# Optimization experiments

Measured on AMD Instinct MI355X. Metric: run time of the kernel, lower is better.

The kernel has to match this reference:

```python
import jax, jax.numpy as jnp
import numpy as np

B, S, V, E = 64, 100, 20000, 128
U, I = 10000, 20000


def setup_inputs() -> dict:
    key = jax.random.key(0)
    ks = jax.random.split(key, 12)
    initrange = 0.1
    return {
        "attr_item": jax.random.randint(ks[0], (B, S), 0, V, dtype=jnp.int32),
        "attr_tf_item": jax.random.uniform(ks[1], (B, S), dtype=jnp.float32),
        "attr_lens_item": jax.random.randint(ks[2], (B,), 1, S + 1, dtype=jnp.int32),
        "item_ids": jax.random.randint(ks[3], (B,), 0, I, dtype=jnp.int32),
        "attr_user": jax.random.randint(ks[4], (B, S), 0, V, dtype=jnp.int32),
        "attr_tf_user": jax.random.uniform(ks[5], (B, S), dtype=jnp.float32),
        "attr_lens_user": jax.random.randint(ks[6], (B,), 1, S + 1, dtype=jnp.int32),
        "user_ids": jax.random.randint(ks[7], (B,), 0, U, dtype=jnp.int32),
        "W_item": jax.random.uniform(ks[8], (V, E), jnp.float32, -initrange, initrange),
        "W_user": jax.random.uniform(ks[9], (V, E), jnp.float32, -initrange, initrange),
        "user_emb": jax.random.uniform(ks[10], (U, E), jnp.float32, -initrange, initrange),
        "item_emb": jax.random.uniform(ks[11], (I, E), jnp.float32, -initrange, initrange),
    }


def _cluster_logits(attr_ids, attr_tf, attr_lens, W):
    # attr_ids: [B,S] int, attr_tf: [B,S] float, attr_lens: [B] int, W: [V,E]
    seq = attr_ids.shape[1]
    mask = (jnp.arange(seq)[None, :] < attr_lens[:, None]).astype(attr_tf.dtype)  # [B,S]
    emb = W[attr_ids]                                   # [B,S,E]
    scores = jnp.einsum("bse,ve->bsv", emb, W)          # [B,S,V]
    cw = jax.nn.softmax(scores, axis=1)                 # softmax over seq dim (dim=1 in torch)
    # Algebraically identical to the [B,S,V,E] broadcast-mul-sum in the original:
    # logits[b,v] = sum_s (tf*mask)[b,s] * cw[b,s,v] * scores[b,s,v]
    return jnp.einsum("bs,bsv,bsv->bv", attr_tf * mask, cw, scores)


def reference(attr_item, attr_tf_item, attr_lens_item, item_ids,
              attr_user, attr_tf_user, attr_lens_user, user_ids,
              W_item, W_user, user_emb, item_emb):
    logits = _cluster_logits(attr_item, attr_tf_item, attr_lens_item, W_item)
    logits = logits + _cluster_logits(attr_user, attr_tf_user, attr_lens_user, W_user)
    logits = logits + user_emb[user_ids] @ W_user.T     # [B,V]
    logits = logits + item_emb[item_ids] @ W_item.T     # [B,V]
    return logits
```

## Files before the change

kernel.cpp:

```cpp
#include <hip/hip_runtime.h>

#define VDIM 20000
#define EDIM 128
#define BATCH 64
#define SEQ 100
#define BN 96
#define NVT 209

typedef float f32x4 __attribute__((ext_vector_type(4)));
typedef short bf16x8 __attribute__((ext_vector_type(8)));
typedef unsigned short ushortx8 __attribute__((ext_vector_type(8)));

typedef __attribute__((address_space(1))) const unsigned int gas_u32;
typedef __attribute__((address_space(3))) unsigned int las_u32;

__device__ __forceinline__ void async16(unsigned short* lds, const unsigned short* g) {
  __builtin_amdgcn_global_load_lds((gas_u32*)g, (las_u32*)lds, 16, 0, 0);
}

__device__ __forceinline__ unsigned short f2bf(float f) {
  unsigned u = __builtin_bit_cast(unsigned, f);
  u += 0x7FFFu + ((u >> 16) & 1u);
  return (unsigned short)(u >> 16);
}

__global__ void prep_kernel(const float* __restrict__ Wi, const float* __restrict__ Wu,
                            const int* __restrict__ attr_item, const int* __restrict__ attr_user,
                            const int* __restrict__ item_ids, const int* __restrict__ user_ids,
                            const float* __restrict__ item_emb, const float* __restrict__ user_emb,
                            unsigned short* __restrict__ wbf, unsigned short* __restrict__ abf) {
  const int bid = blockIdx.x, t = threadIdx.x;
  if (bid < 2500) {
    const int c = bid & 1;
    const float* src = c ? Wu : Wi;
    unsigned short* dst = wbf + (size_t)c * (VDIM * EDIM);
    const int i0 = ((bid >> 1) * 256 + t) * 8;
    float4 a = *(const float4*)(src + i0);
    float4 b = *(const float4*)(src + i0 + 4);
    ushortx8 o;
    o[0] = f2bf(a.x); o[1] = f2bf(a.y); o[2] = f2bf(a.z); o[3] = f2bf(a.w);
    o[4] = f2bf(b.x); o[5] = f2bf(b.y); o[6] = f2bf(b.z); o[7] = f2bf(b.w);
    *(ushortx8*)(dst + i0) = o;
  } else {
    const int g = bid - 2500;
    const int b = g & 63, c = g >> 6;
    const int r = t >> 1, h = t & 1;
    const int* ids = c ? attr_user : attr_item;
    const float* W = c ? Wu : Wi;
    const float* demb = c ? user_emb : item_emb;
    const int* dids = c ? user_ids : item_ids;
    unsigned short* dst = abf + (size_t)(c * BATCH + b) * 16384;
    const float* src = nullptr;
    if (r < SEQ)       src = W + (size_t)ids[b * SEQ + r] * EDIM;
    else if (r == SEQ) src = demb + (size_t)dids[b] * EDIM;
    if (src) {
      #pragma unroll
      for (int k = 0; k < 8; ++k) {
        const int jj = h * 8 + k;
        const int j = jj ^ (r & 15);
        float4 a  = *(const float4*)(src + j * 8);
        float4 bb = *(const float4*)(src + j * 8 + 4);
        ushortx8 o;
        o[0] = f2bf(a.x);  o[1] = f2bf(a.y);  o[2] = f2bf(a.z);  o[3] = f2bf(a.w);
        o[4] = f2bf(bb.x); o[5] = f2bf(bb.y); o[6] = f2bf(bb.z); o[7] = f2bf(bb.w);
        *(ushortx8*)(dst + (r * 16 + jj) * 8) = o;
      }
    } else {
      ushortx8 z = {0, 0, 0, 0, 0, 0, 0, 0};
      #pragma unroll
      for (int k = 0; k < 8; ++k) *(ushortx8*)(dst + (r * 16 + h * 8 + k) * 8) = z;
    }
  }
}

__global__ __launch_bounds__(256, 3)
void main_kernel(const unsigned short* __restrict__ wbf, const unsigned short* __restrict__ abf,
                 const float* __restrict__ tf_item, const int* __restrict__ lens_item,
                 const float* __restrict__ tf_user, const int* __restrict__ lens_user,
                 float* __restrict__ out) {
  __shared__ __align__(16) unsigned short sA[16384];
  __shared__ float sDen[2][2][BN];
  __shared__ float sNum[2][2][BN];
  __shared__ float sDir[2][BN];
  __shared__ float sTF[2][4][128];
  __shared__ int   sLen[2][4];
  __shared__ float sRes[4][BN];

  const int t = threadIdx.x;
  const int v0 = blockIdx.x * BN;
  const int bg4 = blockIdx.y * 4;
  const int lane = t & 63, wave = t >> 6;
  const int wm = wave >> 1, wn = wave & 1;
  const int quad = lane >> 4, l15 = lane & 15;

  #pragma unroll
  for (int k = t; k < 1024; k += 256) {
    const int c = k >> 9, bi = (k >> 7) & 3, si = k & 127;
    float w = 0.f;
    if (si < SEQ) w = (c ? tf_user : tf_item)[(bg4 + bi) * SEQ + si];
    sTF[c][bi][si] = w;
  }
  if (t < 8) sLen[t >> 2][t & 3] = ((t >= 4) ? lens_user : lens_item)[bg4 + (t & 3)];

  bf16x8 breg[3][4];
  #pragma unroll
  for (int nt = 0; nt < 3; ++nt) {
    const int v = v0 + wn * 48 + nt * 16 + l15;
    const unsigned short* p = wbf + (size_t)v * EDIM + quad * 8;
    const bool ok = (v < VDIM);
    #pragma unroll
    for (int ks = 0; ks < 4; ++ks) {
      bf16x8 z = {0, 0, 0, 0, 0, 0, 0, 0};
      breg[nt][ks] = ok ? *(const bf16x8*)(p + ks * 32) : z;
    }
  }

  {
    const unsigned short* gb = abf + (size_t)bg4 * 16384;
    #pragma unroll
    for (int i = 0; i < 8; ++i)
      async16(&sA[(i * 256 + wave * 64) * 8], gb + (size_t)(i * 256 + t) * 8);
  }

  #pragma unroll 1
  for (int s = 0; s < 8; ++s) {
    const int c = s >> 2, it = s & 3, buf = s & 1;

    __syncthreads();

    if (s > 0 && t < BN) {
      const int ps = s - 1, p = ps & 1, pit = ps & 3;
      float den = sDen[p][0][t] + sDen[p][1][t];
      float num = sNum[p][0][t] + sNum[p][1][t];
      const float dir = sDir[p][t];
      den -= 11.f + __expf(dir);
      const float val = num * __builtin_amdgcn_rcpf(den) + dir;
      if (ps < 4) sRes[pit][t] = val;
      else {
        const int v = v0 + t;
        if (v < VDIM) out[(size_t)(bg4 + pit) * VDIM + v] = sRes[pit][t] + val;
      }
    }

    f32x4 acc[4][3];
    #pragma unroll
    for (int mt = 0; mt < 4; ++mt)
      #pragma unroll
      for (int nt = 0; nt < 3; ++nt) { f32x4 z = {0.f, 0.f, 0.f, 0.f}; acc[mt][nt] = z; }

    const unsigned char* pA = (const unsigned char*)&sA[0];
    #pragma unroll
    for (int ks = 0; ks < 4; ++ks) {
      const int j = ks * 4 + quad;
      const int sw = ((j ^ l15) << 4);
      bf16x8 af[4];
      #pragma unroll
      for (int mt = 0; mt < 4; ++mt)
        af[mt] = *(const bf16x8*)(pA + (wm * 64 + mt * 16 + l15) * 256 + sw);
      #pragma unroll
      for (int mt = 0; mt < 4; ++mt)
        #pragma unroll
        for (int nt = 0; nt < 3; ++nt)
          acc[mt][nt] = __builtin_amdgcn_mfma_f32_16x16x32_bf16(af[mt], breg[nt][ks], acc[mt][nt], 0, 0, 0);
    }

    __syncthreads();

    if (s < 7) {
      const int ns = s + 1;
      const unsigned short* gb = abf + (size_t)((ns >> 2) * BATCH + bg4 + (ns & 3)) * 16384;
      #pragma unroll
      for (int i = 0; i < 8; ++i)
        async16(&sA[(i * 256 + wave * 64) * 8], gb + (size_t)(i * 256 + t) * 8);
    }
    if (s == 3) {
      const unsigned short* wb1 = wbf + (size_t)VDIM * EDIM;
      #pragma unroll
      for (int nt = 0; nt < 3; ++nt) {
        const int v = v0 + wn * 48 + nt * 16 + l15;
        const unsigned short* p = wb1 + (size_t)v * EDIM + quad * 8;
        const bool ok = (v < VDIM);
        #pragma unroll
        for (int ks = 0; ks < 4; ++ks) {
          bf16x8 z = {0, 0, 0, 0, 0, 0, 0, 0};
          breg[nt][ks] = ok ? *(const bf16x8*)(p + ks * 32) : z;
        }
      }
    }

    const int lenb = sLen[c][it];
    float wv[4][4];
    #pragma unroll
    for (int mt = 0; mt < 4; ++mt)
      #pragma unroll
      for (int r = 0; r < 4; ++r) {
        const int row = wm * 64 + mt * 16 + quad * 4 + r;
        wv[mt][r] = (row < lenb) ? sTF[c][it][row & 127] : 0.f;
      }

    #pragma unroll
    for (int nt = 0; nt < 3; ++nt) {
      float den = 0.f, num = 0.f;
      #pragma unroll
      for (int mt = 0; mt < 3; ++mt)
        #pragma unroll
        for (int r = 0; r < 4; ++r) {
          const float v = acc[mt][nt][r];
          const float e = __expf(v);
          den += e;
          num = fmaf(wv[mt][r], e * v, num);
        }
      if (wm == 0) {
        #pragma unroll
        for (int r = 0; r < 4; ++r) {
          const float v = acc[3][nt][r];
          const float e = __expf(v);
          den += e;
          num = fmaf(wv[3][r], e * v, num);
        }
      }
      den += __shfl_xor(den, 16, 64);
      den += __shfl_xor(den, 32, 64);
      num += __shfl_xor(num, 16, 64);
      num += __shfl_xor(num, 32, 64);
      const int col = wn * 48 + nt * 16 + l15;
      if (quad == 0) {
        sDen[buf][wm][col] = den;
        sNum[buf][wm][col] = num;
      }
      if (wm == 1 && quad == 1) sDir[buf][col] = acc[2][nt][0];
    }
  }

  __syncthreads();

  if (t < BN) {
    float den = sDen[1][0][t] + sDen[1][1][t];
    float num = sNum[1][0][t] + sNum[1][1][t];
    const float dir = sDir[1][t];
    den -= 11.f + __expf(dir);
    const float val = num * __builtin_amdgcn_rcpf(den) + dir;
    const int v = v0 + t;
    if (v < VDIM) out[(size_t)(bg4 + 3) * VDIM + v] = sRes[3][t] + val;
  }
}

extern "C" void kernel_launch(void* const* d_in, const int* in_sizes, int n_in,
                              void* d_out, int out_size, void* d_ws, size_t ws_size,
                              hipStream_t stream) {
  const int*   attr_item = (const int*)d_in[0];
  const float* tf_item   = (const float*)d_in[1];
  const int*   lens_item = (const int*)d_in[2];
  const int*   item_ids  = (const int*)d_in[3];
  const int*   attr_user = (const int*)d_in[4];
  const float* tf_user   = (const float*)d_in[5];
  const int*   lens_user = (const int*)d_in[6];
  const int*   user_ids  = (const int*)d_in[7];
  const float* W_item    = (const float*)d_in[8];
  const float* W_user    = (const float*)d_in[9];
  const float* user_emb  = (const float*)d_in[10];
  const float* item_emb  = (const float*)d_in[11];
  float* out = (float*)d_out;

  unsigned short* wbf = (unsigned short*)d_ws;
  unsigned short* abf = wbf + (size_t)2 * VDIM * EDIM;

  prep_kernel<<<dim3(2500 + 128), 256, 0, stream>>>(W_item, W_user, attr_item, attr_user,
                                                    item_ids, user_ids, item_emb, user_emb,
                                                    wbf, abf);
  main_kernel<<<dim3(NVT, 16), 256, 0, stream>>>(wbf, abf, tf_item, lens_item,
                                                 tf_user, lens_user, out);
}
```

Measured before the change: 242.0 us.

## Convert W to bf16 inside main kernel and shrink vocab tile and A tile

Drops the separate whole-W bf16 conversion pass: main_kernel now loads fp32 W rows and converts them to bf16 in registers. The vocab tile shrinks from 96 to 64 columns, giving more blocks, and occupancy is raised to 4 blocks per CU. The A tile is trimmed to 112 rows, the prep grid is split across halves, and the tf weights are read straight from global memory instead of staged in LDS. The main cost is that each W row is now read in fp32 and converted again by every one of the 16 batch-group blocks, which doubles W read bytes.

```diff
diff --git a/kernel.cpp b/kernel.cpp
--- a/kernel.cpp
+++ b/kernel.cpp
@@ -4,8 +4,10 @@
 #define EDIM 128
 #define BATCH 64
 #define SEQ 100
-#define BN 96
-#define NVT 209
+#define BN 64
+#define NVT 313
+#define AROWS 112
+#define ATILE (AROWS * EDIM)
 
 typedef float f32x4 __attribute__((ext_vector_type(4)));
 typedef short bf16x8 __attribute__((ext_vector_type(8)));
@@ -28,63 +30,51 @@
                             const int* __restrict__ attr_item, const int* __restrict__ attr_user,
                             const int* __restrict__ item_ids, const int* __restrict__ user_ids,
                             const float* __restrict__ item_emb, const float* __restrict__ user_emb,
-                            unsigned short* __restrict__ wbf, unsigned short* __restrict__ abf) {
-  const int bid = blockIdx.x, t = threadIdx.x;
-  if (bid < 2500) {
-    const int c = bid & 1;
-    const float* src = c ? Wu : Wi;
-    unsigned short* dst = wbf + (size_t)c * (VDIM * EDIM);
-    const int i0 = ((bid >> 1) * 256 + t) * 8;
-    float4 a = *(const float4*)(src + i0);
-    float4 b = *(const float4*)(src + i0 + 4);
-    ushortx8 o;
-    o[0] = f2bf(a.x); o[1] = f2bf(a.y); o[2] = f2bf(a.z); o[3] = f2bf(a.w);
-    o[4] = f2bf(b.x); o[5] = f2bf(b.y); o[6] = f2bf(b.z); o[7] = f2bf(b.w);
-    *(ushortx8*)(dst + i0) = o;
+                            unsigned short* __restrict__ abf) {
+  const int g = blockIdx.x;
+  const int b = g & 63, c = (g >> 6) & 1, half = g >> 7;
+  const int t = threadIdx.x;
+  const int r = t >> 1, h = t & 1;
+  if (r >= AROWS) return;
+  const int* ids = c ? attr_user : attr_item;
+  const float* W = c ? Wu : Wi;
+  const float* demb = c ? user_emb : item_emb;
+  const int* dids = c ? user_ids : item_ids;
+  unsigned short* dst = abf + (size_t)(c * BATCH + b) * ATILE;
+  const float* src = nullptr;
+  if (r < SEQ)       src = W + (size_t)ids[b * SEQ + r] * EDIM;
+  else if (r == SEQ) src = demb + (size_t)dids[b] * EDIM;
+  if (src) {
+    #pragma unroll
+    for (int k = 0; k < 4; ++k) {
+      const int jj = h * 8 + half * 4 + k;
+      const int j = jj ^ (r & 15);
+      float4 a  = *(const float4*)(src + j * 8);
+      float4 bb = *(const float4*)(src + j * 8 + 4);
+      ushortx8 o;
+      o[0] = f2bf(a.x);  o[1] = f2bf(a.y);  o[2] = f2bf(a.z);  o[3] = f2bf(a.w);
+      o[4] = f2bf(bb.x); o[5] = f2bf(bb.y); o[6] = f2bf(bb.z); o[7] = f2bf(bb.w);
+      *(ushortx8*)(dst + (r * 16 + jj) * 8) = o;
+    }
   } else {
-    const int g = bid - 2500;
-    const int b = g & 63, c = g >> 6;
-    const int r = t >> 1, h = t & 1;
-    const int* ids = c ? attr_user : attr_item;
-    const float* W = c ? Wu : Wi;
-    const float* demb = c ? user_emb : item_emb;
-    const int* dids = c ? user_ids : item_ids;
-    unsigned short* dst = abf + (size_t)(c * BATCH + b) * 16384;
-    const float* src = nullptr;
-    if (r < SEQ)       src = W + (size_t)ids[b * SEQ + r] * EDIM;
-    else if (r == SEQ) src = demb + (size_t)dids[b] * EDIM;
-    if (src) {
-      #pragma unroll
-      for (int k = 0; k < 8; ++k) {
-        const int jj = h * 8 + k;
-        const int j = jj ^ (r & 15);
-        float4 a  = *(const float4*)(src + j * 8);
-        float4 bb = *(const float4*)(src + j * 8 + 4);
-        ushortx8 o;
-        o[0] = f2bf(a.x);  o[1] = f2bf(a.y);  o[2] = f2bf(a.z);  o[3] = f2bf(a.w);
-        o[4] = f2bf(bb.x); o[5] = f2bf(bb.y); o[6] = f2bf(bb.z); o[7] = f2bf(bb.w);
-        *(ushortx8*)(dst + (r * 16 + jj) * 8) = o;
-      }
-    } else {
-      ushortx8 z = {0, 0, 0, 0, 0, 0, 0, 0};
-      #pragma unroll
-      for (int k = 0; k < 8; ++k) *(ushortx8*)(dst + (r * 16 + h * 8 + k) * 8) = z;
-    }
-  }
-}
-
-__global__ __launch_bounds__(256, 3)
-void main_kernel(const unsigned short* __restrict__ wbf, const unsigned short* __restrict__ abf,
+    ushortx8 z = {0, 0, 0, 0, 0, 0, 0, 0};
+    #pragma unroll
+    for (int k = 0; k < 4; ++k) *(ushortx8*)(dst + (r * 16 + h * 8 + half * 4 + k) * 8) = z;
+  }
+}
+
+__global__ __launch_bounds__(256, 4)
+void main_kernel(const float* __restrict__ Wi, const float* __restrict__ Wu,
+                 const unsigned short* __restrict__ abf,
                  const float* __restrict__ tf_item, const int* __restrict__ lens_item,
                  const float* __restrict__ tf_user, const int* __restrict__ lens_user,
                  float* __restrict__ out) {
-  __shared__ __align__(16) unsigned short sA[16384];
+  __shared__ __align__(16) unsigned short sA[ATILE];
   __shared__ float sDen[2][2][BN];
   __shared__ float sNum[2][2][BN];
   __shared__ float sDir[2][BN];
-  __shared__ float sTF[2][4][128];
+  __shared__ float sRes[4][BN];
   __shared__ int   sLen[2][4];
-  __shared__ float sRes[4][BN];
 
   const int t = threadIdx.x;
   const int v0 = blockIdx.x * BN;
@@ -93,32 +83,32 @@
   const int wm = wave >> 1, wn = wave & 1;
   const int quad = lane >> 4, l15 = lane & 15;
 
-  #pragma unroll
-  for (int k = t; k < 1024; k += 256) {
-    const int c = k >> 9, bi = (k >> 7) & 3, si = k & 127;
-    float w = 0.f;
-    if (si < SEQ) w = (c ? tf_user : tf_item)[(bg4 + bi) * SEQ + si];
-    sTF[c][bi][si] = w;
-  }
   if (t < 8) sLen[t >> 2][t & 3] = ((t >= 4) ? lens_user : lens_item)[bg4 + (t & 3)];
 
-  bf16x8 breg[3][4];
-  #pragma unroll
-  for (int nt = 0; nt < 3; ++nt) {
-    const int v = v0 + wn * 48 + nt * 16 + l15;
-    const unsigned short* p = wbf + (size_t)v * EDIM + quad * 8;
-    const bool ok = (v < VDIM);
-    #pragma unroll
-    for (int ks = 0; ks < 4; ++ks) {
-      bf16x8 z = {0, 0, 0, 0, 0, 0, 0, 0};
-      breg[nt][ks] = ok ? *(const bf16x8*)(p + ks * 32) : z;
-    }
-  }
-
+  bf16x8 breg[2][4];
   {
-    const unsigned short* gb = abf + (size_t)bg4 * 16384;
-    #pragma unroll
-    for (int i = 0; i < 8; ++i)
+    #pragma unroll
+    for (int nt = 0; nt < 2; ++nt) {
+      const int v = v0 + wn * 32 + nt * 16 + l15;
+      const bool ok = (v < VDIM);
+      const float* p = Wi + (size_t)(ok ? v : 0) * EDIM + quad * 8;
+      #pragma unroll
+      for (int ks = 0; ks < 4; ++ks) {
+        float4 x = *(const float4*)(p + ks * 32);
+        float4 y = *(const float4*)(p + ks * 32 + 4);
+        ushortx8 o;
+        o[0] = f2bf(x.x); o[1] = f2bf(x.y); o[2] = f2bf(x.z); o[3] = f2bf(x.w);
+        o[4] = f2bf(y.x); o[5] = f2bf(y.y); o[6] = f2bf(y.z); o[7] = f2bf(y.w);
+        ushortx8 z = {0, 0, 0, 0, 0, 0, 0, 0};
+        breg[nt][ks] = __builtin_bit_cast(bf16x8, ok ? o : z);
+      }
+    }
+  }
+
+  {
+    const unsigned short* gb = abf + (size_t)bg4 * ATILE;
+    #pragma unroll
+    for (int i = 0; i < 7; ++i)
       async16(&sA[(i * 256 + wave * 64) * 8], gb + (size_t)(i * 256 + t) * 8);
   }
 
@@ -142,64 +132,78 @@
       }
     }
 
-    f32x4 acc[4][3];
+    const int lenb = sLen[c][it];
+    const float* tfp = (c ? tf_user : tf_item) + (size_t)(bg4 + it) * SEQ;
+    float wv[4][4];
+    #pragma unroll
+    for (int mt = 0; mt < 4; ++mt) {
+      const int row0 = wm * 64 + mt * 16 + quad * 4;
+      float4 tfv = {0.f, 0.f, 0.f, 0.f};
+      if (row0 < SEQ) tfv = *(const float4*)(tfp + row0);
+      wv[mt][0] = (row0 + 0 < lenb) ? tfv.x : 0.f;
+      wv[mt][1] = (row0 + 1 < lenb) ? tfv.y : 0.f;
+      wv[mt][2] = (row0 + 2 < lenb) ? tfv.z : 0.f;
+      wv[mt][3] = (row0 + 3 < lenb) ? tfv.w : 0.f;
+    }
+
+    f32x4 acc[4][2];
     #pragma unroll
     for (int mt = 0; mt < 4; ++mt)
       #pragma unroll
-      for (int nt = 0; nt < 3; ++nt) { f32x4 z = {0.f, 0.f, 0.f, 0.f}; acc[mt][nt] = z; }
+      for (int nt = 0; nt < 2; ++nt) { f32x4 z = {0.f, 0.f, 0.f, 0.f}; acc[mt][nt] = z; }
 
     const unsigned char* pA = (const unsigned char*)&sA[0];
     #pragma unroll
     for (int ks = 0; ks < 4; ++ks) {
       const int j = ks * 4 + quad;
       const int sw = ((j ^ l15) << 4);
-      bf16x8 af[4];
-      #pragma unroll
-      for (int mt = 0; mt < 4; ++mt)
+      bf16x8 af[3];
+      #pragma unroll
+      for (int mt = 0; mt < 3; ++mt)
         af[mt] = *(const bf16x8*)(pA + (wm * 64 + mt * 16 + l15) * 256 + sw);
       #pragma unroll
-      for (int mt = 0; mt < 4; ++mt)
-        #pragma unroll
-        for (int nt = 0; nt < 3; ++nt)
+      for (int mt = 0; mt < 3; ++mt)
+        #pragma unroll
+        for (int nt = 0; nt < 2; ++nt)
           acc[mt][nt] = __builtin_amdgcn_mfma_f32_16x16x32_bf16(af[mt], breg[nt][ks], acc[mt][nt], 0, 0, 0);
+      if (wm == 0) {
+        const bf16x8 a3 = *(const bf16x8*)(pA + (3 * 16 + l15) * 256 + sw);
+        #pragma unroll
+        for (int nt = 0; nt < 2; ++nt)
+          acc[3][nt] = __builtin_amdgcn_mfma_f32_16x16x32_bf16(a3, breg[nt][ks], acc[3][nt], 0, 0, 0);
+      }
     }
 
     __syncthreads();
 
     if (s < 7) {
       const int ns = s + 1;
-      const unsigned short* gb = abf + (size_t)((ns >> 2) * BATCH + bg4 + (ns & 3)) * 16384;
-      #pragma unroll
-      for (int i = 0; i < 8; ++i)
+      const unsigned short* gb = abf + (size_t)((ns >> 2) * BATCH + bg4 + (ns & 3)) * ATILE;
+      #pragma unroll
+      for (int i = 0; i < 7; ++i)
         async16(&sA[(i * 256 + wave * 64) * 8], gb + (size_t)(i * 256 + t) * 8);
     }
     if (s == 3) {
-      const unsigned short* wb1 = wbf + (size_t)VDIM * EDIM;
-      #pragma unroll
-      for (int nt = 0; nt < 3; ++nt) {
-        const int v = v0 + wn * 48 + nt * 16 + l15;
-        const unsigned short* p = wb1 + (size_t)v * EDIM + quad * 8;
+      #pragma unroll
+      for (int nt = 0; nt < 2; ++nt) {
+        const int v = v0 + wn * 32 + nt * 16 + l15;
         const bool ok = (v < VDIM);
+        const float* p = Wu + (size_t)(ok ? v : 0) * EDIM + quad * 8;
         #pragma unroll
         for (int ks = 0; ks < 4; ++ks) {
-          bf16x8 z = {0, 0, 0, 0, 0, 0, 0, 0};
-          breg[nt][ks] = ok ? *(const bf16x8*)(p + ks * 32) : z;
+          float4 x = *(const float4*)(p + ks * 32);
+          float4 y = *(const float4*)(p + ks * 32 + 4);
+          ushortx8 o;
+          o[0] = f2bf(x.x); o[1] = f2bf(x.y); o[2] = f2bf(x.z); o[3] = f2bf(x.w);
+          o[4] = f2bf(y.x); o[5] = f2bf(y.y); o[6] = f2bf(y.z); o[7] = f2bf(y.w);
+          ushortx8 z = {0, 0, 0, 0, 0, 0, 0, 0};
+          breg[nt][ks] = __builtin_bit_cast(bf16x8, ok ? o : z);
         }
       }
     }
 
-    const int lenb = sLen[c][it];
-    float wv[4][4];
-    #pragma unroll
-    for (int mt = 0; mt < 4; ++mt)
-      #pragma unroll
-      for (int r = 0; r < 4; ++r) {
-        const int row = wm * 64 + mt * 16 + quad * 4 + r;
-        wv[mt][r] = (row < lenb) ? sTF[c][it][row & 127] : 0.f;
-      }
-
-    #pragma unroll
-    for (int nt = 0; nt < 3; ++nt) {
+    #pragma unroll
+    for (int nt = 0; nt < 2; ++nt) {
       float den = 0.f, num = 0.f;
       #pragma unroll
       for (int mt = 0; mt < 3; ++mt)
@@ -223,7 +227,7 @@
       den += __shfl_xor(den, 32, 64);
       num += __shfl_xor(num, 16, 64);
       num += __shfl_xor(num, 32, 64);
-      const int col = wn * 48 + nt * 16 + l15;
+      const int col = wn * 32 + nt * 16 + l15;
       if (quad == 0) {
         sDen[buf][wm][col] = den;
         sNum[buf][wm][col] = num;
@@ -262,12 +266,10 @@
   const float* item_emb  = (const float*)d_in[11];
   float* out = (float*)d_out;
 
-  unsigned short* wbf = (unsigned short*)d_ws;
-  unsigned short* abf = wbf + (size_t)2 * VDIM * EDIM;
-
-  prep_kernel<<<dim3(2500 + 128), 256, 0, stream>>>(W_item, W_user, attr_item, attr_user,
-                                                    item_ids, user_ids, item_emb, user_emb,
-                                                    wbf, abf);
-  main_kernel<<<dim3(NVT, 16), 256, 0, stream>>>(wbf, abf, tf_item, lens_item,
+  unsigned short* abf = (unsigned short*)d_ws;
+
+  prep_kernel<<<dim3(256), 256, 0, stream>>>(W_item, W_user, attr_item, attr_user,
+                                             item_ids, user_ids, item_emb, user_emb, abf);
+  main_kernel<<<dim3(NVT, 16), 256, 0, stream>>>(W_item, W_user, abf, tf_item, lens_item,
                                                  tf_user, lens_user, out);
 }
```

New measurement: 268.0 us. +10.8%, slower.

## Trim A tile to 112 rows, skip dead MFMA rows, raise occupancy to 4

Applied to the files above, without the earlier changes.

The A tile is shrunk from 128 to 112 rows, since rows past 100 plus the direct-embedding row are zero padding. This cuts the staging writes, the async copies (7 chunks instead of 8) and LDS use. Wave-row group 1 now skips the fourth M-tile of MFMAs, whose rows only held padding. The shared TF table is dropped in favour of direct float4 global loads of the tf weights, and launch bounds are raised to 4 blocks per CU. The trade-off is more register pressure from the higher occupancy target, plus uncached global loads inside the epilogue.

```diff
diff --git a/kernel.cpp b/kernel.cpp
--- a/kernel.cpp
+++ b/kernel.cpp
@@ -6,6 +6,8 @@
 #define SEQ 100
 #define BN 96
 #define NVT 209
+#define AROWS 112
+#define ATILE (AROWS * EDIM)
 
 typedef float f32x4 __attribute__((ext_vector_type(4)));
 typedef short bf16x8 __attribute__((ext_vector_type(8)));
@@ -45,11 +47,12 @@
     const int g = bid - 2500;
     const int b = g & 63, c = g >> 6;
     const int r = t >> 1, h = t & 1;
+    if (r >= AROWS) return;
     const int* ids = c ? attr_user : attr_item;
     const float* W = c ? Wu : Wi;
     const float* demb = c ? user_emb : item_emb;
     const int* dids = c ? user_ids : item_ids;
-    unsigned short* dst = abf + (size_t)(c * BATCH + b) * 16384;
+    unsigned short* dst = abf + (size_t)(c * BATCH + b) * ATILE;
     const float* src = nullptr;
     if (r < SEQ)       src = W + (size_t)ids[b * SEQ + r] * EDIM;
     else if (r == SEQ) src = demb + (size_t)dids[b] * EDIM;
@@ -73,18 +76,17 @@
   }
 }
 
-__global__ __launch_bounds__(256, 3)
+__global__ __launch_bounds__(256, 4)
 void main_kernel(const unsigned short* __restrict__ wbf, const unsigned short* __restrict__ abf,
                  const float* __restrict__ tf_item, const int* __restrict__ lens_item,
                  const float* __restrict__ tf_user, const int* __restrict__ lens_user,
                  float* __restrict__ out) {
-  __shared__ __align__(16) unsigned short sA[16384];
+  __shared__ __align__(16) unsigned short sA[ATILE];
   __shared__ float sDen[2][2][BN];
   __shared__ float sNum[2][2][BN];
   __shared__ float sDir[2][BN];
-  __shared__ float sTF[2][4][128];
+  __shared__ float sRes[4][BN];
   __shared__ int   sLen[2][4];
-  __shared__ float sRes[4][BN];
 
   const int t = threadIdx.x;
   const int v0 = blockIdx.x * BN;
@@ -93,13 +95,6 @@
   const int wm = wave >> 1, wn = wave & 1;
   const int quad = lane >> 4, l15 = lane & 15;
 
-  #pragma unroll
-  for (int k = t; k < 1024; k += 256) {
-    const int c = k >> 9, bi = (k >> 7) & 3, si = k & 127;
-    float w = 0.f;
-    if (si < SEQ) w = (c ? tf_user : tf_item)[(bg4 + bi) * SEQ + si];
-    sTF[c][bi][si] = w;
-  }
   if (t < 8) sLen[t >> 2][t & 3] = ((t >= 4) ? lens_user : lens_item)[bg4 + (t & 3)];
 
   bf16x8 breg[3][4];
@@ -116,9 +111,9 @@
   }
 
   {
-    const unsigned short* gb = abf + (size_t)bg4 * 16384;
-    #pragma unroll
-    for (int i = 0; i < 8; ++i)
+    const unsigned short* gb = abf + (size_t)bg4 * ATILE;
+    #pragma unroll
+    for (int i = 0; i < 7; ++i)
       async16(&sA[(i * 256 + wave * 64) * 8], gb + (size_t)(i * 256 + t) * 8);
   }
 
@@ -153,24 +148,30 @@
     for (int ks = 0; ks < 4; ++ks) {
       const int j = ks * 4 + quad;
       const int sw = ((j ^ l15) << 4);
-      bf16x8 af[4];
-      #pragma unroll
-      for (int mt = 0; mt < 4; ++mt)
+      bf16x8 af[3];
+      #pragma unroll
+      for (int mt = 0; mt < 3; ++mt)
         af[mt] = *(const bf16x8*)(pA + (wm * 64 + mt * 16 + l15) * 256 + sw);
       #pragma unroll
-      for (int mt = 0; mt < 4; ++mt)
+      for (int mt = 0; mt < 3; ++mt)
         #pragma unroll
         for (int nt = 0; nt < 3; ++nt)
           acc[mt][nt] = __builtin_amdgcn_mfma_f32_16x16x32_bf16(af[mt], breg[nt][ks], acc[mt][nt], 0, 0, 0);
+      if (wm == 0) {
+        const bf16x8 a3 = *(const bf16x8*)(pA + (3 * 16 + l15) * 256 + sw);
+        #pragma unroll
+        for (int nt = 0; nt < 3; ++nt)
+          acc[3][nt] = __builtin_amdgcn_mfma_f32_16x16x32_bf16(a3, breg[nt][ks], acc[3][nt], 0, 0, 0);
+      }
     }
 
     __syncthreads();
 
     if (s < 7) {
       const int ns = s + 1;
-      const unsigned short* gb = abf + (size_t)((ns >> 2) * BATCH + bg4 + (ns & 3)) * 16384;
-      #pragma unroll
-      for (int i = 0; i < 8; ++i)
+      const unsigned short* gb = abf + (size_t)((ns >> 2) * BATCH + bg4 + (ns & 3)) * ATILE;
+      #pragma unroll
+      for (int i = 0; i < 7; ++i)
         async16(&sA[(i * 256 + wave * 64) * 8], gb + (size_t)(i * 256 + t) * 8);
     }
     if (s == 3) {
@@ -189,36 +190,51 @@
     }
 
     const int lenb = sLen[c][it];
-    float wv[4][4];
-    #pragma unroll
-    for (int mt = 0; mt < 4; ++mt)
-      #pragma unroll
-      for (int r = 0; r < 4; ++r) {
-        const int row = wm * 64 + mt * 16 + quad * 4 + r;
-        wv[mt][r] = (row < lenb) ? sTF[c][it][row & 127] : 0.f;
-      }
-
-    #pragma unroll
-    for (int nt = 0; nt < 3; ++nt) {
-      float den = 0.f, num = 0.f;
-      #pragma unroll
-      for (int mt = 0; mt < 3; ++mt)
+    const float* tfp = (c ? tf_user : tf_item) + (size_t)(bg4 + it) * SEQ;
+    float dens[3] = {0.f, 0.f, 0.f};
+    float nums[3] = {0.f, 0.f, 0.f};
+    #pragma unroll
+    for (int mt = 0; mt < 3; ++mt) {
+      const int row0 = wm * 64 + mt * 16 + quad * 4;
+      float4 tfv = {0.f, 0.f, 0.f, 0.f};
+      if (row0 < SEQ) tfv = *(const float4*)(tfp + row0);
+      float wv[4];
+      wv[0] = (row0 + 0 < lenb) ? tfv.x : 0.f;
+      wv[1] = (row0 + 1 < lenb) ? tfv.y : 0.f;
+      wv[2] = (row0 + 2 < lenb) ? tfv.z : 0.f;
+      wv[3] = (row0 + 3 < lenb) ? tfv.w : 0.f;
+      #pragma unroll
+      for (int nt = 0; nt < 3; ++nt)
         #pragma unroll
         for (int r = 0; r < 4; ++r) {
           const float v = acc[mt][nt][r];
           const float e = __expf(v);
-          den += e;
-          num = fmaf(wv[mt][r], e * v, num);
+          dens[nt] += e;
+          nums[nt] = fmaf(wv[r], e * v, nums[nt]);
         }
-      if (wm == 0) {
+    }
+    if (wm == 0) {
+      const int row0 = 3 * 16 + quad * 4;
+      float4 tfv = *(const float4*)(tfp + row0);
+      float wv[4];
+      wv[0] = (row0 + 0 < lenb) ? tfv.x : 0.f;
+      wv[1] = (row0 + 1 < lenb) ? tfv.y : 0.f;
+      wv[2] = (row0 + 2 < lenb) ? tfv.z : 0.f;
+      wv[3] = (row0 + 3 < lenb) ? tfv.w : 0.f;
+      #pragma unroll
+      for (int nt = 0; nt < 3; ++nt)
         #pragma unroll
         for (int r = 0; r < 4; ++r) {
           const float v = acc[3][nt][r];
           const float e = __expf(v);
-          den += e;
-          num = fmaf(wv[3][r], e * v, num);
+          dens[nt] += e;
+          nums[nt] = fmaf(wv[r], e * v, nums[nt]);
         }
-      }
+    }
+
+    #pragma unroll
+    for (int nt = 0; nt < 3; ++nt) {
+      float den = dens[nt], num = nums[nt];
       den += __shfl_xor(den, 16, 64);
       den += __shfl_xor(den, 32, 64);
       num += __shfl_xor(num, 16, 64);
```

After: 441.6 us. 1.83x slower.

## Shrink tiles to 64 columns, trim A tile to 112 rows, swizzle grid

Applied to the files above, without the earlier changes.

Cuts the vocabulary tile from 96 to 64 columns and the staged A tile from 128 to 112 rows, so LDS use and MFMA work on padded rows both drop. Wave row-group 1 skips the fourth M sub-tile, and occupancy is raised to 4 blocks per CU. Blocks are remapped with a 1D grid and an XCD-aware index so that blocks sharing a batch group or vocabulary slice tend to land on the same XCD. The trade-off is that each block reuses every A tile over fewer columns, so total A traffic rises and more blocks are launched.

```diff
diff --git a/kernel.cpp b/kernel.cpp
--- a/kernel.cpp
+++ b/kernel.cpp
@@ -4,8 +4,12 @@
 #define EDIM 128
 #define BATCH 64
 #define SEQ 100
-#define BN 96
-#define NVT 209
+#define BN 64
+#define NVT 313
+#define AROWS 112
+#define ATILE (AROWS * EDIM)
+#define GRID (NVT * 16)
+#define GPX (GRID / 8)
 
 typedef float f32x4 __attribute__((ext_vector_type(4)));
 typedef short bf16x8 __attribute__((ext_vector_type(8)));
@@ -45,11 +49,12 @@
     const int g = bid - 2500;
     const int b = g & 63, c = g >> 6;
     const int r = t >> 1, h = t & 1;
+    if (r >= AROWS) return;
     const int* ids = c ? attr_user : attr_item;
     const float* W = c ? Wu : Wi;
     const float* demb = c ? user_emb : item_emb;
     const int* dids = c ? user_ids : item_ids;
-    unsigned short* dst = abf + (size_t)(c * BATCH + b) * 16384;
+    unsigned short* dst = abf + (size_t)(c * BATCH + b) * ATILE;
     const float* src = nullptr;
     if (r < SEQ)       src = W + (size_t)ids[b * SEQ + r] * EDIM;
     else if (r == SEQ) src = demb + (size_t)dids[b] * EDIM;
@@ -73,12 +78,12 @@
   }
 }
 
-__global__ __launch_bounds__(256, 3)
+__global__ __launch_bounds__(256, 4)
 void main_kernel(const unsigned short* __restrict__ wbf, const unsigned short* __restrict__ abf,
                  const float* __restrict__ tf_item, const int* __restrict__ lens_item,
                  const float* __restrict__ tf_user, const int* __restrict__ lens_user,
                  float* __restrict__ out) {
-  __shared__ __align__(16) unsigned short sA[16384];
+  __shared__ __align__(16) unsigned short sA[ATILE];
   __shared__ float sDen[2][2][BN];
   __shared__ float sNum[2][2][BN];
   __shared__ float sDir[2][BN];
@@ -87,8 +92,10 @@
   __shared__ float sRes[4][BN];
 
   const int t = threadIdx.x;
-  const int v0 = blockIdx.x * BN;
-  const int bg4 = blockIdx.y * 4;
+  const int bid = blockIdx.x;
+  const int p = (bid & 7) * GPX + (bid >> 3);
+  const int v0 = (p >> 4) * BN;
+  const int bg4 = (p & 15) * 4;
   const int lane = t & 63, wave = t >> 6;
   const int wm = wave >> 1, wn = wave & 1;
   const int quad = lane >> 4, l15 = lane & 15;
@@ -102,23 +109,23 @@
   }
   if (t < 8) sLen[t >> 2][t & 3] = ((t >= 4) ? lens_user : lens_item)[bg4 + (t & 3)];
 
-  bf16x8 breg[3][4];
+  bf16x8 breg[2][4];
   #pragma unroll
-  for (int nt = 0; nt < 3; ++nt) {
-    const int v = v0 + wn * 48 + nt * 16 + l15;
-    const unsigned short* p = wbf + (size_t)v * EDIM + quad * 8;
+  for (int nt = 0; nt < 2; ++nt) {
+    const int v = v0 + wn * 32 + nt * 16 + l15;
+    const unsigned short* pb = wbf + (size_t)v * EDIM + quad * 8;
     const bool ok = (v < VDIM);
     #pragma unroll
     for (int ks = 0; ks < 4; ++ks) {
       bf16x8 z = {0, 0, 0, 0, 0, 0, 0, 0};
-      breg[nt][ks] = ok ? *(const bf16x8*)(p + ks * 32) : z;
+      breg[nt][ks] = ok ? *(const bf16x8*)(pb + ks * 32) : z;
     }
   }
 
   {
-    const unsigned short* gb = abf + (size_t)bg4 * 16384;
-    #pragma unroll
-    for (int i = 0; i < 8; ++i)
+    const unsigned short* gb = abf + (size_t)bg4 * ATILE;
+    #pragma unroll
+    for (int i = 0; i < 7; ++i)
       async16(&sA[(i * 256 + wave * 64) * 8], gb + (size_t)(i * 256 + t) * 8);
   }
 
@@ -129,10 +136,10 @@
     __syncthreads();
 
     if (s > 0 && t < BN) {
-      const int ps = s - 1, p = ps & 1, pit = ps & 3;
-      float den = sDen[p][0][t] + sDen[p][1][t];
-      float num = sNum[p][0][t] + sNum[p][1][t];
-      const float dir = sDir[p][t];
+      const int ps = s - 1, pp = ps & 1, pit = ps & 3;
+      float den = sDen[pp][0][t] + sDen[pp][1][t];
+      float num = sNum[pp][0][t] + sNum[pp][1][t];
+      const float dir = sDir[pp][t];
       den -= 11.f + __expf(dir);
       const float val = num * __builtin_amdgcn_rcpf(den) + dir;
       if (ps < 4) sRes[pit][t] = val;
@@ -142,48 +149,54 @@
       }
     }
 
-    f32x4 acc[4][3];
+    f32x4 acc[4][2];
     #pragma unroll
     for (int mt = 0; mt < 4; ++mt)
       #pragma unroll
-      for (int nt = 0; nt < 3; ++nt) { f32x4 z = {0.f, 0.f, 0.f, 0.f}; acc[mt][nt] = z; }
+      for (int nt = 0; nt < 2; ++nt) { f32x4 z = {0.f, 0.f, 0.f, 0.f}; acc[mt][nt] = z; }
 
     const unsigned char* pA = (const unsigned char*)&sA[0];
     #pragma unroll
     for (int ks = 0; ks < 4; ++ks) {
       const int j = ks * 4 + quad;
       const int sw = ((j ^ l15) << 4);
-      bf16x8 af[4];
-      #pragma unroll
-      for (int mt = 0; mt < 4; ++mt)
+      bf16x8 af[3];
+      #pragma unroll
+      for (int mt = 0; mt < 3; ++mt)
         af[mt] = *(const bf16x8*)(pA + (wm * 64 + mt * 16 + l15) * 256 + sw);
       #pragma unroll
-      for (int mt = 0; mt < 4; ++mt)
-        #pragma unroll
-        for (int nt = 0; nt < 3; ++nt)
+      for (int mt = 0; mt < 3; ++mt)
+        #pragma unroll
+        for (int nt = 0; nt < 2; ++nt)
           acc[mt][nt] = __builtin_amdgcn_mfma_f32_16x16x32_bf16(af[mt], breg[nt][ks], acc[mt][nt], 0, 0, 0);
+      if (wm == 0) {
+        const bf16x8 a3 = *(const bf16x8*)(pA + (3 * 16 + l15) * 256 + sw);
+        #pragma unroll
+        for (int nt = 0; nt < 2; ++nt)
+          acc[3][nt] = __builtin_amdgcn_mfma_f32_16x16x32_bf16(a3, breg[nt][ks], acc[3][nt], 0, 0, 0);
+      }
     }
 
     __syncthreads();
 
     if (s < 7) {
       const int ns = s + 1;
-      const unsigned short* gb = abf + (size_t)((ns >> 2) * BATCH + bg4 + (ns & 3)) * 16384;
-      #pragma unroll
-      for (int i = 0; i < 8; ++i)
+      const unsigned short* gb = abf + (size_t)((ns >> 2) * BATCH + bg4 + (ns & 3)) * ATILE;
+      #pragma unroll
+      for (int i = 0; i < 7; ++i)
         async16(&sA[(i * 256 + wave * 64) * 8], gb + (size_t)(i * 256 + t) * 8);
     }
     if (s == 3) {
       const unsigned short* wb1 = wbf + (size_t)VDIM * EDIM;
       #pragma unroll
-      for (int nt = 0; nt < 3; ++nt) {
-        const int v = v0 + wn * 48 + nt * 16 + l15;
-        const unsigned short* p = wb1 + (size_t)v * EDIM + quad * 8;
+      for (int nt = 0; nt < 2; ++nt) {
+        const int v = v0 + wn * 32 + nt * 16 + l15;
+        const unsigned short* pb = wb1 + (size_t)v * EDIM + quad * 8;
         const bool ok = (v < VDIM);
         #pragma unroll
         for (int ks = 0; ks < 4; ++ks) {
           bf16x8 z = {0, 0, 0, 0, 0, 0, 0, 0};
-          breg[nt][ks] = ok ? *(const bf16x8*)(p + ks * 32) : z;
+          breg[nt][ks] = ok ? *(const bf16x8*)(pb + ks * 32) : z;
         }
       }
     }
@@ -199,7 +212,7 @@
       }
 
     #pragma unroll
-    for (int nt = 0; nt < 3; ++nt) {
+    for (int nt = 0; nt < 2; ++nt) {
       float den = 0.f, num = 0.f;
       #pragma unroll
       for (int mt = 0; mt < 3; ++mt)
@@ -223,7 +236,7 @@
       den += __shfl_xor(den, 32, 64);
       num += __shfl_xor(num, 16, 64);
       num += __shfl_xor(num, 32, 64);
-      const int col = wn * 48 + nt * 16 + l15;
+      const int col = wn * 32 + nt * 16 + l15;
       if (quad == 0) {
         sDen[buf][wm][col] = den;
         sNum[buf][wm][col] = num;
@@ -268,6 +281,6 @@
   prep_kernel<<<dim3(2500 + 128), 256, 0, stream>>>(W_item, W_user, attr_item, attr_user,
                                                     item_ids, user_ids, item_emb, user_emb,
                                                     wbf, abf);
-  main_kernel<<<dim3(NVT, 16), 256, 0, stream>>>(wbf, abf, tf_item, lens_item,
-                                                 tf_user, lens_user, out);
-}
+  main_kernel<<<dim3(GRID), 256, 0, stream>>>(wbf, abf, tf_item, lens_item,
+                                              tf_user, lens_user, out);
+}
```

Result: no change. 243.4 us (+0.6%).
